# Optimization experiments

Measured on AMD Instinct MI355X. Metric: run time of the kernel, lower is better.

## Reference

```python
import jax, jax.numpy as jnp
import numpy as np

B, S, E, H = 4, 2048, 1024, 16
D = E // H  # key_size


def setup_inputs() -> dict:
    key = jax.random.key(0)
    ks = jax.random.split(key, 6)
    s = 1.0 / np.sqrt(E)
    return {
        "X": jax.random.normal(ks[0], (B, S, E), dtype=jnp.float32),
        "Wq": jax.random.uniform(ks[1], (E, E), jnp.float32, -s, s),
        "Wk": jax.random.uniform(ks[2], (E, E), jnp.float32, -s, s),
        "Wv": jax.random.uniform(ks[3], (E, E), jnp.float32, -s, s),
        "Wo": jax.random.uniform(ks[4], (E, E), jnp.float32, -s, s),
        "bo": jax.random.uniform(ks[5], (E,), jnp.float32, -s, s),
    }


def reference(X, Wq, Wk, Wv, Wo, bo):
    # Linear layers: y = x @ W^T (torch convention), no bias for q/k/v
    def split(x):  # [B,S,E] -> [B,H,S,D]
        return x.reshape(B, S, H, D).transpose(0, 2, 1, 3)

    q = split(X @ Wq.T)
    k = split(X @ Wk.T)
    v = split(X @ Wv.T)
    scale = jnp.asarray(np.sqrt(D), dtype=X.dtype)
    scores = jnp.einsum("bhqd,bhkd->bhqk", q, k) / scale
    probs = jax.nn.softmax(scores, axis=-1)
    ctx = jnp.einsum("bhqk,bhkd->bhqd", probs, v)
    out = ctx.transpose(0, 2, 1, 3).reshape(B, S, E)
    return out @ Wo.T + bo
```

## Files before the change

kernel.cpp:

```cpp
#include <hip/hip_runtime.h>
#include <hip/hip_bf16.h>

typedef short bf16x8 __attribute__((ext_vector_type(8)));
typedef float f32x4  __attribute__((ext_vector_type(4)));

__device__ __forceinline__ short f2bf(float f) {
    union { float f; unsigned u; } x; x.f = f;
    unsigned r = x.u + 0x7fffu + ((x.u >> 16) & 1u);
    return (short)(r >> 16);
}

__device__ __forceinline__ unsigned rbits(float f) {
    union { float f; unsigned u; } x; x.f = f;
    return x.u + 0x8000u;
}
__device__ __forceinline__ int pack2(float a, float b) {
    return (int)__builtin_amdgcn_perm(rbits(b), rbits(a), 0x07060302u);
}

__device__ __forceinline__ f32x4 mfma32k(bf16x8 a, bf16x8 b, f32x4 c) {
    return __builtin_amdgcn_mfma_f32_16x16x32_bf16(a, b, c, 0, 0, 0);
}

#define GLDS16(g, l)                                                            \
    __builtin_amdgcn_global_load_lds(                                           \
        (const __attribute__((address_space(1))) void*)(g),                     \
        (__attribute__((address_space(3))) void*)(l), 16, 0, 0)

static constexpr int Bb = 4, Ss = 2048, Ee = 1024, Hh = 16, Dd = 64;
static constexpr int Mrows = Bb * Ss;
static constexpr float CL2 = 0.1803368801111204f;

__global__ void cvt_all(const float* __restrict__ X,  const float* __restrict__ Wq,
                        const float* __restrict__ Wk, const float* __restrict__ Wv,
                        const float* __restrict__ Wo,
                        short* __restrict__ Xb, short* __restrict__ Wqk,
                        short* __restrict__ Wvb, short* __restrict__ Wob) {
    int bid = blockIdx.x;
    const float* src; short* dst; int off; float scale = 1.0f;
    if (bid < 8192) {
        src = X; dst = Xb; off = bid * 1024;
    } else {
        int wsel = (bid - 8192) >> 10;
        off = ((bid - 8192) & 1023) * 1024;
        if      (wsel == 0) { src = Wq; dst = Wqk;                scale = CL2; }
        else if (wsel == 1) { src = Wk; dst = Wqk + Ee * Ee; }
        else if (wsel == 2) { src = Wv; dst = Wvb; }
        else                { src = Wo; dst = Wob; }
    }
    int i = off + threadIdx.x * 4;
    float4 v = *(const float4*)(src + i);
    short4 o;
    o.x = f2bf(v.x * scale); o.y = f2bf(v.y * scale);
    o.z = f2bf(v.z * scale); o.w = f2bf(v.w * scale);
    *(short4*)(dst + i) = o;
}

__device__ __forceinline__ void gemm_pipe_256x128(
    short* lds, const short* hA, const short* hB,
    int wv, int lane16, int wn, int fsw0, int fsw1, int aoff,
    f32x4 (&acc)[8][2])
{
#define STG(gsrc, matOff, half, j, T, buf)                                      \
    GLDS16((gsrc) + ((half) * 128 + (j) * 64) * 1024 + (T) * 64,                \
           lds + (buf) * 32768 + (matOff) + (half) * 8192 + (j) * 4096 + wv * 512)

    STG(hA, 0,     0, 0, 0, 0); STG(hA, 0,     0, 1, 0, 0);
    STG(hA, 0,     1, 0, 0, 0); STG(hA, 0,     1, 1, 0, 0);
    STG(hB, 16384, 0, 0, 0, 0); STG(hB, 16384, 0, 1, 0, 0);
    STG(hA, 0,     0, 0, 1, 1); STG(hA, 0,     0, 1, 1, 1);
    asm volatile("s_waitcnt vmcnt(2)" ::: "memory");
    __builtin_amdgcn_s_barrier();

    const int bvoff = (wn * 32 + lane16) * 64;
    for (int T = 0; T < 16; ++T) {
        const int cur = T & 1, nxt = cur ^ 1;
        const short* sAc = lds + cur * 32768;
        const short* sBc = sAc + 16384;
        bf16x8 bb[2][2];
#pragma unroll
        for (int nj = 0; nj < 2; ++nj) {
            bb[nj][0] = *(const bf16x8*)(sBc + bvoff + nj * 1024 + fsw0);
            bb[nj][1] = *(const bf16x8*)(sBc + bvoff + nj * 1024 + fsw1);
        }
        bf16x8 a0, a1, a2, a3, a4, a5, a6, a7;
        a0 = *(const bf16x8*)(sAc + aoff + 0 * 1024 + fsw0);
        a1 = *(const bf16x8*)(sAc + aoff + 0 * 1024 + fsw1);
        a2 = *(const bf16x8*)(sAc + aoff + 1 * 1024 + fsw0);
        a3 = *(const bf16x8*)(sAc + aoff + 1 * 1024 + fsw1);
        a4 = *(const bf16x8*)(sAc + aoff + 2 * 1024 + fsw0);
        a5 = *(const bf16x8*)(sAc + aoff + 2 * 1024 + fsw1);
        a6 = *(const bf16x8*)(sAc + aoff + 3 * 1024 + fsw0);
        a7 = *(const bf16x8*)(sAc + aoff + 3 * 1024 + fsw1);
        if (T < 15) {
            STG(hA, 0,     1, 0, T + 1, nxt); STG(hA, 0,     1, 1, T + 1, nxt);
            STG(hB, 16384, 0, 0, T + 1, nxt); STG(hB, 16384, 0, 1, T + 1, nxt);
        }
        __builtin_amdgcn_s_barrier();
        __builtin_amdgcn_s_setprio(1);
#pragma unroll
        for (int nj = 0; nj < 2; ++nj) {
            acc[0][nj] = mfma32k(a0, bb[nj][0], acc[0][nj]);
            acc[0][nj] = mfma32k(a1, bb[nj][1], acc[0][nj]);
            acc[1][nj] = mfma32k(a2, bb[nj][0], acc[1][nj]);
            acc[1][nj] = mfma32k(a3, bb[nj][1], acc[1][nj]);
            acc[2][nj] = mfma32k(a4, bb[nj][0], acc[2][nj]);
            acc[2][nj] = mfma32k(a5, bb[nj][1], acc[2][nj]);
            acc[3][nj] = mfma32k(a6, bb[nj][0], acc[3][nj]);
            acc[3][nj] = mfma32k(a7, bb[nj][1], acc[3][nj]);
        }
        __builtin_amdgcn_s_setprio(0);
        __builtin_amdgcn_s_barrier();
        a0 = *(const bf16x8*)(sAc + aoff + 4 * 1024 + fsw0);
        a1 = *(const bf16x8*)(sAc + aoff + 4 * 1024 + fsw1);
        a2 = *(const bf16x8*)(sAc + aoff + 5 * 1024 + fsw0);
        a3 = *(const bf16x8*)(sAc + aoff + 5 * 1024 + fsw1);
        a4 = *(const bf16x8*)(sAc + aoff + 6 * 1024 + fsw0);
        a5 = *(const bf16x8*)(sAc + aoff + 6 * 1024 + fsw1);
        a6 = *(const bf16x8*)(sAc + aoff + 7 * 1024 + fsw0);
        a7 = *(const bf16x8*)(sAc + aoff + 7 * 1024 + fsw1);
        __builtin_amdgcn_s_barrier();
        __builtin_amdgcn_s_setprio(1);
#pragma unroll
        for (int nj = 0; nj < 2; ++nj) {
            acc[4][nj] = mfma32k(a0, bb[nj][0], acc[4][nj]);
            acc[4][nj] = mfma32k(a1, bb[nj][1], acc[4][nj]);
            acc[5][nj] = mfma32k(a2, bb[nj][0], acc[5][nj]);
            acc[5][nj] = mfma32k(a3, bb[nj][1], acc[5][nj]);
            acc[6][nj] = mfma32k(a4, bb[nj][0], acc[6][nj]);
            acc[6][nj] = mfma32k(a5, bb[nj][1], acc[6][nj]);
            acc[7][nj] = mfma32k(a6, bb[nj][0], acc[7][nj]);
            acc[7][nj] = mfma32k(a7, bb[nj][1], acc[7][nj]);
        }
        __builtin_amdgcn_s_setprio(0);
        __builtin_amdgcn_s_barrier();
        if (T < 14) {
            STG(hA, 0, 0, 0, T + 2, cur); STG(hA, 0, 0, 1, T + 2, cur);
            asm volatile("s_waitcnt vmcnt(2)" ::: "memory");
            __builtin_amdgcn_s_barrier();
        } else if (T == 14) {
            asm volatile("s_waitcnt vmcnt(0)" ::: "memory");
            __builtin_amdgcn_s_barrier();
        }
    }
#undef STG
}

__global__ __launch_bounds__(512, 2)
void gemm_fused(const short* __restrict__ A0, const short* __restrict__ B0,
                short* __restrict__ C0,
                const short* __restrict__ A1, const short* __restrict__ B1,
                short* __restrict__ C1) {
    __shared__ __align__(16) short lds[65536];
    const int t = threadIdx.x, l = t & 63, wv = t >> 6;
    const int lane16 = l & 15, quad = l >> 4;
    const int wm = wv >> 2, wn = wv & 3;

    int bid = blockIdx.x;
    int wg = (bid & 7) * 32 + (bid >> 3);
    const int bm = wg & 31, bn = wg >> 5;

    const int grow = t >> 3;
    const int lsl  = ((t & 7) ^ ((t >> 3) & 7)) * 8;
    const short* gA = A0 + (size_t)(bm * 256 + grow) * 1024 + lsl;
    const short* gB = B0 + (size_t)(bn * 256 + grow) * 1024 + lsl;

#define STAGE8(gsrc, matOff, half, j, T, buf)                                   \
    GLDS16((gsrc) + ((half) * 128 + (j) * 64) * 1024 + (T) * 64,                \
           lds + (buf) * 32768 + (matOff) + (half) * 8192 + (j) * 4096 + wv * 512)

    const int fsw0 = ((quad)     ^ (lane16 & 7)) * 8;
    const int fsw1 = ((quad + 4) ^ (lane16 & 7)) * 8;
    const int aoff = (wm * 128 + lane16) * 64;
    const int boff = (wn * 64  + lane16) * 64;

    f32x4 acc[8][4] = {};

    STAGE8(gA, 0,     0, 0, 0, 0); STAGE8(gA, 0,     0, 1, 0, 0);
    STAGE8(gA, 0,     1, 0, 0, 0); STAGE8(gA, 0,     1, 1, 0, 0);
    STAGE8(gB, 16384, 0, 0, 0, 0); STAGE8(gB, 16384, 0, 1, 0, 0);
    STAGE8(gB, 16384, 1, 0, 0, 0); STAGE8(gB, 16384, 1, 1, 0, 0);
    STAGE8(gA, 0,     0, 0, 1, 1); STAGE8(gA, 0,     0, 1, 1, 1);
    asm volatile("s_waitcnt vmcnt(2)" ::: "memory");
    __builtin_amdgcn_s_barrier();

#define ARD(MI0)                                                                \
    a0 = *(const bf16x8*)(sAc + aoff + (MI0) * 1024 + fsw0);                    \
    a1 = *(const bf16x8*)(sAc + aoff + (MI0) * 1024 + fsw1);                    \
    a2 = *(const bf16x8*)(sAc + aoff + ((MI0) + 1) * 1024 + fsw0);              \
    a3 = *(const bf16x8*)(sAc + aoff + ((MI0) + 1) * 1024 + fsw1);

#define MFQ(MI0)                                                                \
    __builtin_amdgcn_s_setprio(1);                                              \
    _Pragma("unroll")                                                           \
    for (int nj = 0; nj < 4; ++nj) {                                            \
        acc[MI0][nj]       = mfma32k(a0, bf[nj][0], acc[MI0][nj]);              \
        acc[MI0][nj]       = mfma32k(a1, bf[nj][1], acc[MI0][nj]);              \
        acc[(MI0) + 1][nj] = mfma32k(a2, bf[nj][0], acc[(MI0) + 1][nj]);        \
        acc[(MI0) + 1][nj] = mfma32k(a3, bf[nj][1], acc[(MI0) + 1][nj]);        \
    }                                                                           \
    __builtin_amdgcn_s_setprio(0);

    for (int T = 0; T < 16; ++T) {
        const int cur = T & 1, nxt = cur ^ 1;
        const short* sAc = lds + cur * 32768;
        const short* sBc = sAc + 16384;
        bf16x8 bf[4][2];
#pragma unroll
        for (int nj = 0; nj < 4; ++nj) {
            bf[nj][0] = *(const bf16x8*)(sBc + boff + nj * 1024 + fsw0);
            bf[nj][1] = *(const bf16x8*)(sBc + boff + nj * 1024 + fsw1);
        }
        bf16x8 a0, a1, a2, a3;
        ARD(0)
        if (T < 15) { STAGE8(gA, 0, 1, 0, T + 1, nxt); STAGE8(gA, 0, 1, 1, T + 1, nxt); }
        __builtin_amdgcn_s_barrier();
        MFQ(0)
        __builtin_amdgcn_s_barrier();
        ARD(2)
        if (T < 15) { STAGE8(gB, 16384, 0, 0, T + 1, nxt); STAGE8(gB, 16384, 0, 1, T + 1, nxt); }
        __builtin_amdgcn_s_barrier();
        MFQ(2)
        __builtin_amdgcn_s_barrier();
        ARD(4)
        if (T < 15) { STAGE8(gB, 16384, 1, 0, T + 1, nxt); STAGE8(gB, 16384, 1, 1, T + 1, nxt); }
        __builtin_amdgcn_s_barrier();
        MFQ(4)
        __builtin_amdgcn_s_barrier();
        ARD(6)
        __builtin_amdgcn_s_barrier();
        MFQ(6)
        __builtin_amdgcn_s_barrier();
        if (T < 14) {
            STAGE8(gA, 0, 0, 0, T + 2, cur); STAGE8(gA, 0, 0, 1, T + 2, cur);
            asm volatile("s_waitcnt vmcnt(2)" ::: "memory");
            __builtin_amdgcn_s_barrier();
        } else if (T == 14) {
            asm volatile("s_waitcnt vmcnt(0)" ::: "memory");
            __builtin_amdgcn_s_barrier();
        }
    }
#undef ARD
#undef MFQ
#undef STAGE8

#pragma unroll
    for (int mi = 0; mi < 8; ++mi)
#pragma unroll
        for (int nj = 0; nj < 4; ++nj) {
            int row = bm * 256 + wm * 128 + mi * 16 + quad * 4;
            int col = bn * 256 + wn * 64 + nj * 16 + lane16;
#pragma unroll
            for (int r = 0; r < 4; ++r)
                C0[(size_t)(row + r) * 2048 + col] = f2bf(acc[mi][nj][r]);
        }

    const int vbm = wg & 3, vbn = wg >> 2;
    const short* hA = A1 + (size_t)(vbm * 256 + grow) * 1024 + lsl;
    const short* hB = B1 + (size_t)(vbn * 128 + grow) * 1024 + lsl;
    f32x4 accB[8][2] = {};
    gemm_pipe_256x128(lds, hA, hB, wv, lane16, wn, fsw0, fsw1, aoff, accB);

    const int sEven = (lane16 >> 2) * 8 + (lane16 & 3);
#pragma unroll
    for (int mi = 0; mi < 8; ++mi)
#pragma unroll
        for (int nj = 0; nj < 2; ++nj) {
            int row = vbm * 256 + wm * 128 + mi * 16 + quad * 4;
            int col = vbn * 128 + wn * 32 + nj * 16 + lane16;
            col = (col & ~31) | (sEven + (nj & 1) * 4);
#pragma unroll
            for (int r = 0; r < 4; ++r)
                C1[(size_t)(row + r) * 8192 + col] = f2bf(accB[mi][nj][r]);
        }
}

__global__ __launch_bounds__(512, 2)
void gemm_out(const short* __restrict__ A, const short* __restrict__ Bm,
              float* __restrict__ C, const float* __restrict__ bias) {
    __shared__ __align__(16) short lds[65536];
    const int t = threadIdx.x, l = t & 63, wv = t >> 6;
    const int lane16 = l & 15, quad = l >> 4;
    const int wm = wv >> 2, wn = wv & 3;

    int bid = blockIdx.x;
    int wg = (bid & 7) * 32 + (bid >> 3);
    const int bm = wg >> 3, bn = wg & 7;

    const int grow = t >> 3;
    const int lsl  = ((t & 7) ^ ((t >> 3) & 7)) * 8;
    const short* hA = A  + (size_t)(bm * 256 + grow) * 1024 + lsl;
    const short* hB = Bm + (size_t)(bn * 128 + grow) * 1024 + lsl;

    const int fsw0 = ((quad)     ^ (lane16 & 7)) * 8;
    const int fsw1 = ((quad + 4) ^ (lane16 & 7)) * 8;
    const int aoff = (wm * 128 + lane16) * 64;

    f32x4 acc[8][2] = {};
    gemm_pipe_256x128(lds, hA, hB, wv, lane16, wn, fsw0, fsw1, aoff, acc);

#pragma unroll
    for (int mi = 0; mi < 8; ++mi)
#pragma unroll
        for (int nj = 0; nj < 2; ++nj) {
            int row = bm * 256 + wm * 128 + mi * 16 + quad * 4;
            int col = bn * 128 + wn * 32 + nj * 16 + lane16;
            float bv = bias[col];
#pragma unroll
            for (int r = 0; r < 4; ++r)
                C[(size_t)(row + r) * 1024 + col] = acc[mi][nj][r] + bv;
        }
}

__global__ __launch_bounds__(256, 4)
void attn_kernel(const short* __restrict__ QK, const short* __restrict__ VT,
                 short* __restrict__ CTX, int bh0) {
    __shared__ __align__(16) short sK[8192];
    __shared__ __align__(16) short sV[8192];
    const int t = threadIdx.x, w = t >> 6, l = t & 63;
    const int lane16 = l & 15, quad = l >> 4;
    const int bh = blockIdx.x + bh0, qt = blockIdx.y;
    const int b = bh >> 4, h = bh & 15;

    const int qx8 = (quad ^ ((lane16 >> 1) & 3)) * 8;

    const short* Qb = QK + ((size_t)(b * 2048 + qt * 128)) * 2048 + h * 64;
    const short* Vb = VT + ((size_t)(h * 64)) * 8192 + (size_t)b * 2048;
    const int ldsOff = (w * 64) * 8;

    int off_kq[4], off_v[4];
#pragma unroll
    for (int p = 0; p < 4; ++p) {
        int c = p * 256 + t;
        int sw = ((c & 3) ^ ((c >> 3) & 3)) * 8;
        off_kq[p] = ((c >> 2) & 127) * 2048 + (c >> 9) * 32 + sw;
        off_v[p]  = ((c >> 2) & 63) * 8192 + (c >> 8) * 32 + sw;
    }

#pragma unroll
    for (int p = 0; p < 4; ++p)
        GLDS16(Qb + off_kq[p], sK + p * 2048 + ldsOff);
    __syncthreads();
    bf16x8 qf[2][2];
#pragma unroll
    for (int mt = 0; mt < 2; ++mt)
#pragma unroll
        for (int ks = 0; ks < 2; ++ks)
            qf[mt][ks] = *(const bf16x8*)(sK + ks * 4096 + (w * 32 + mt * 16 + lane16) * 32 + qx8);
    __syncthreads();

    const short one = (short)0x3F80;
    const bf16x8 ONE8 = {one, one, one, one, one, one, one, one};
    f32x4 lacc[2] = {};
    f32x4 o[2][4] = {};

    const short* kptr = QK + ((size_t)(b * 2048)) * 2048 + 1024 + h * 64;
    const short* vptr = Vb;

    auto QKB = [&](int a, f32x4 (&sc)[2][2]) {
        __builtin_amdgcn_s_setprio(1);
#pragma unroll
        for (int sub = 0; sub < 2; ++sub) {
            int nt = a * 2 + sub;
            bf16x8 kf0 = *(const bf16x8*)(sK + (nt * 16 + lane16) * 32 + qx8);
            bf16x8 kf1 = *(const bf16x8*)(sK + 4096 + (nt * 16 + lane16) * 32 + qx8);
#pragma unroll
            for (int mt = 0; mt < 2; ++mt) {
                f32x4 z = {};
                z = mfma32k(kf0, qf[mt][0], z);
                z = mfma32k(kf1, qf[mt][1], z);
                sc[mt][sub] = z;
            }
        }
        __builtin_amdgcn_s_setprio(0);
    };
    auto PVB = [&](int a, f32x4 (&sc)[2][2]) {
        bf16x8 pf[2];
#pragma unroll
        for (int mt = 0; mt < 2; ++mt) {
            union { int i[4]; bf16x8 v; } u;
#pragma unroll
            for (int sub = 0; sub < 2; ++sub) {
                f32x4 e;
#pragma unroll
                for (int r = 0; r < 4; ++r)
                    e[r] = __builtin_amdgcn_exp2f(sc[mt][sub][r]);
                u.i[sub * 2]     = pack2(e[0], e[1]);
                u.i[sub * 2 + 1] = pack2(e[2], e[3]);
            }
            pf[mt] = u.v;
        }
        __builtin_amdgcn_s_setprio(1);
#pragma unroll
        for (int mt = 0; mt < 2; ++mt)
            lacc[mt] = mfma32k(pf[mt], ONE8, lacc[mt]);
#pragma unroll
        for (int dt = 0; dt < 4; ++dt) {
            bf16x8 vf = *(const bf16x8*)(sV + a * 2048 + (dt * 16 + lane16) * 32 + qx8);
#pragma unroll
            for (int mt = 0; mt < 2; ++mt)
                o[mt][dt] = mfma32k(pf[mt], vf, o[mt][dt]);
        }
        __builtin_amdgcn_s_setprio(0);
    };

    for (int kt = 0; kt < 16; ++kt) {
#pragma unroll
        for (int p = 0; p < 4; ++p)
            GLDS16(kptr + off_kq[p], sK + p * 2048 + ldsOff);
#pragma unroll
        for (int p = 0; p < 4; ++p)
            GLDS16(vptr + off_v[p], sV + p * 2048 + ldsOff);
        kptr += (size_t)128 * 2048;
        vptr += 128;
        __syncthreads();

        f32x4 scA[2][2], scB[2][2];
        QKB(0, scA);
        QKB(1, scB);  PVB(0, scA);
        QKB(2, scA);  PVB(1, scB);
        QKB(3, scB);  PVB(2, scA);
                      PVB(3, scB);
        __syncthreads();
    }

#pragma unroll
    for (int mt = 0; mt < 2; ++mt)
#pragma unroll
        for (int r = 0; r < 4; ++r) {
            float inv = 1.0f / lacc[mt][r];
            int row = b * 2048 + qt * 128 + w * 32 + mt * 16 + quad * 4 + r;
#pragma unroll
            for (int dt = 0; dt < 4; ++dt)
                CTX[(size_t)row * 1024 + h * 64 + dt * 16 + lane16] = f2bf(o[mt][dt][r] * inv);
        }
}

extern "C" void kernel_launch(void* const* d_in, const int* in_sizes, int n_in,
                              void* d_out, int out_size, void* d_ws, size_t ws_size,
                              hipStream_t stream) {
    const float* X  = (const float*)d_in[0];
    const float* Wq = (const float*)d_in[1];
    const float* Wk = (const float*)d_in[2];
    const float* Wv = (const float*)d_in[3];
    const float* Wo = (const float*)d_in[4];
    const float* bo = (const float*)d_in[5];
    float* out = (float*)d_out;

    char* ws = (char*)d_ws;
    constexpr size_t OFF_XB  = 0;
    constexpr size_t OFF_WQK = OFF_XB  + (size_t)Mrows * Ee * 2;
    constexpr size_t OFF_WV  = OFF_WQK + (size_t)2 * Ee * Ee * 2;
    constexpr size_t OFF_WO  = OFF_WV  + (size_t)Ee * Ee * 2;
    constexpr size_t OFF_QK  = OFF_WO  + (size_t)Ee * Ee * 2;
    constexpr size_t OFF_VT  = OFF_QK  + (size_t)Mrows * 2048 * 2;
    constexpr size_t OFF_CTX = OFF_VT  + (size_t)Ee * Mrows * 2;
    short* Xb   = (short*)(ws + OFF_XB);
    short* Wqk  = (short*)(ws + OFF_WQK);
    short* Wvb  = (short*)(ws + OFF_WV);
    short* Wob  = (short*)(ws + OFF_WO);
    short* QKb  = (short*)(ws + OFF_QK);
    short* VTb  = (short*)(ws + OFF_VT);
    short* CTX  = (short*)(ws + OFF_CTX);

    cvt_all<<<12288, 256, 0, stream>>>(X, Wq, Wk, Wv, Wo, Xb, Wqk, Wvb, Wob);

    gemm_fused<<<256, 512, 0, stream>>>(Xb, Wqk, QKb, Wvb, Xb, VTb);

    attn_kernel<<<dim3(Bb * Hh, Ss / 128), 256, 0, stream>>>(QKb, VTb, CTX, 0);

    gemm_out<<<256, 512, 0, stream>>>(CTX, Wob, out, bo);
}
```

Before: 248.7 us.

## Reshape 256x128 GEMM warp tiling to 4x2 and split attention launch in two

Changes the per-warp tile in the 256x128 GEMM pipeline from 128x32 (8x2 MFMA tiles) to 64x64 (4x4 tiles). Each warp now does fewer LDS A-fragment reads and more B-fragment reuse per stage, giving a more balanced operand load. The epilogues of the fused V projection and the output GEMM are remapped to match. The attention launch is also split into two launches of 32 batch-heads each, which adds launch overhead and has no clear speed rationale.

```diff
diff --git a/kernel.cpp b/kernel.cpp
--- a/kernel.cpp
+++ b/kernel.cpp
@@ -58,8 +58,8 @@
 
 __device__ __forceinline__ void gemm_pipe_256x128(
     short* lds, const short* hA, const short* hB,
-    int wv, int lane16, int wn, int fsw0, int fsw1, int aoff,
-    f32x4 (&acc)[8][2])
+    int wv, int lane16, int fsw0, int fsw1,
+    f32x4 (&acc)[4][4])
 {
 #define STG(gsrc, matOff, half, j, T, buf)                                      \
     GLDS16((gsrc) + ((half) * 128 + (j) * 64) * 1024 + (T) * 64,                \
@@ -72,26 +72,25 @@
     asm volatile("s_waitcnt vmcnt(2)" ::: "memory");
     __builtin_amdgcn_s_barrier();
 
-    const int bvoff = (wn * 32 + lane16) * 64;
+    const int wm2 = wv & 3, wn2 = wv >> 2;
+    const int aoff = (wm2 * 64 + lane16) * 64;
+    const int boff = (wn2 * 64 + lane16) * 64;
+
     for (int T = 0; T < 16; ++T) {
         const int cur = T & 1, nxt = cur ^ 1;
         const short* sAc = lds + cur * 32768;
         const short* sBc = sAc + 16384;
-        bf16x8 bb[2][2];
-#pragma unroll
-        for (int nj = 0; nj < 2; ++nj) {
-            bb[nj][0] = *(const bf16x8*)(sBc + bvoff + nj * 1024 + fsw0);
-            bb[nj][1] = *(const bf16x8*)(sBc + bvoff + nj * 1024 + fsw1);
-        }
-        bf16x8 a0, a1, a2, a3, a4, a5, a6, a7;
+        bf16x8 bb[4][2];
+#pragma unroll
+        for (int nj = 0; nj < 4; ++nj) {
+            bb[nj][0] = *(const bf16x8*)(sBc + boff + nj * 1024 + fsw0);
+            bb[nj][1] = *(const bf16x8*)(sBc + boff + nj * 1024 + fsw1);
+        }
+        bf16x8 a0, a1, a2, a3;
         a0 = *(const bf16x8*)(sAc + aoff + 0 * 1024 + fsw0);
         a1 = *(const bf16x8*)(sAc + aoff + 0 * 1024 + fsw1);
         a2 = *(const bf16x8*)(sAc + aoff + 1 * 1024 + fsw0);
         a3 = *(const bf16x8*)(sAc + aoff + 1 * 1024 + fsw1);
-        a4 = *(const bf16x8*)(sAc + aoff + 2 * 1024 + fsw0);
-        a5 = *(const bf16x8*)(sAc + aoff + 2 * 1024 + fsw1);
-        a6 = *(const bf16x8*)(sAc + aoff + 3 * 1024 + fsw0);
-        a7 = *(const bf16x8*)(sAc + aoff + 3 * 1024 + fsw1);
         if (T < 15) {
             STG(hA, 0,     1, 0, T + 1, nxt); STG(hA, 0,     1, 1, T + 1, nxt);
             STG(hB, 16384, 0, 0, T + 1, nxt); STG(hB, 16384, 0, 1, T + 1, nxt);
@@ -99,38 +98,26 @@
         __builtin_amdgcn_s_barrier();
         __builtin_amdgcn_s_setprio(1);
 #pragma unroll
-        for (int nj = 0; nj < 2; ++nj) {
+        for (int nj = 0; nj < 4; ++nj) {
             acc[0][nj] = mfma32k(a0, bb[nj][0], acc[0][nj]);
             acc[0][nj] = mfma32k(a1, bb[nj][1], acc[0][nj]);
             acc[1][nj] = mfma32k(a2, bb[nj][0], acc[1][nj]);
             acc[1][nj] = mfma32k(a3, bb[nj][1], acc[1][nj]);
-            acc[2][nj] = mfma32k(a4, bb[nj][0], acc[2][nj]);
-            acc[2][nj] = mfma32k(a5, bb[nj][1], acc[2][nj]);
-            acc[3][nj] = mfma32k(a6, bb[nj][0], acc[3][nj]);
-            acc[3][nj] = mfma32k(a7, bb[nj][1], acc[3][nj]);
         }
         __builtin_amdgcn_s_setprio(0);
         __builtin_amdgcn_s_barrier();
-        a0 = *(const bf16x8*)(sAc + aoff + 4 * 1024 + fsw0);
-        a1 = *(const bf16x8*)(sAc + aoff + 4 * 1024 + fsw1);
-        a2 = *(const bf16x8*)(sAc + aoff + 5 * 1024 + fsw0);
-        a3 = *(const bf16x8*)(sAc + aoff + 5 * 1024 + fsw1);
-        a4 = *(const bf16x8*)(sAc + aoff + 6 * 1024 + fsw0);
-        a5 = *(const bf16x8*)(sAc + aoff + 6 * 1024 + fsw1);
-        a6 = *(const bf16x8*)(sAc + aoff + 7 * 1024 + fsw0);
-        a7 = *(const bf16x8*)(sAc + aoff + 7 * 1024 + fsw1);
+        a0 = *(const bf16x8*)(sAc + aoff + 2 * 1024 + fsw0);
+        a1 = *(const bf16x8*)(sAc + aoff + 2 * 1024 + fsw1);
+        a2 = *(const bf16x8*)(sAc + aoff + 3 * 1024 + fsw0);
+        a3 = *(const bf16x8*)(sAc + aoff + 3 * 1024 + fsw1);
         __builtin_amdgcn_s_barrier();
         __builtin_amdgcn_s_setprio(1);
 #pragma unroll
-        for (int nj = 0; nj < 2; ++nj) {
-            acc[4][nj] = mfma32k(a0, bb[nj][0], acc[4][nj]);
-            acc[4][nj] = mfma32k(a1, bb[nj][1], acc[4][nj]);
-            acc[5][nj] = mfma32k(a2, bb[nj][0], acc[5][nj]);
-            acc[5][nj] = mfma32k(a3, bb[nj][1], acc[5][nj]);
-            acc[6][nj] = mfma32k(a4, bb[nj][0], acc[6][nj]);
-            acc[6][nj] = mfma32k(a5, bb[nj][1], acc[6][nj]);
-            acc[7][nj] = mfma32k(a6, bb[nj][0], acc[7][nj]);
-            acc[7][nj] = mfma32k(a7, bb[nj][1], acc[7][nj]);
+        for (int nj = 0; nj < 4; ++nj) {
+            acc[2][nj] = mfma32k(a0, bb[nj][0], acc[2][nj]);
+            acc[2][nj] = mfma32k(a1, bb[nj][1], acc[2][nj]);
+            acc[3][nj] = mfma32k(a2, bb[nj][0], acc[3][nj]);
+            acc[3][nj] = mfma32k(a3, bb[nj][1], acc[3][nj]);
         }
         __builtin_amdgcn_s_setprio(0);
         __builtin_amdgcn_s_barrier();
@@ -258,16 +245,17 @@
     const int vbm = wg & 3, vbn = wg >> 2;
     const short* hA = A1 + (size_t)(vbm * 256 + grow) * 1024 + lsl;
     const short* hB = B1 + (size_t)(vbn * 128 + grow) * 1024 + lsl;
-    f32x4 accB[8][2] = {};
-    gemm_pipe_256x128(lds, hA, hB, wv, lane16, wn, fsw0, fsw1, aoff, accB);
-
+    f32x4 accB[4][4] = {};
+    gemm_pipe_256x128(lds, hA, hB, wv, lane16, fsw0, fsw1, accB);
+
+    const int wm2 = wv & 3, wn2 = wv >> 2;
     const int sEven = (lane16 >> 2) * 8 + (lane16 & 3);
 #pragma unroll
-    for (int mi = 0; mi < 8; ++mi)
-#pragma unroll
-        for (int nj = 0; nj < 2; ++nj) {
-            int row = vbm * 256 + wm * 128 + mi * 16 + quad * 4;
-            int col = vbn * 128 + wn * 32 + nj * 16 + lane16;
+    for (int mi = 0; mi < 4; ++mi)
+#pragma unroll
+        for (int nj = 0; nj < 4; ++nj) {
+            int row = vbm * 256 + wm2 * 64 + mi * 16 + quad * 4;
+            int col = vbn * 128 + wn2 * 64 + nj * 16 + lane16;
             col = (col & ~31) | (sEven + (nj & 1) * 4);
 #pragma unroll
             for (int r = 0; r < 4; ++r)
@@ -281,7 +269,6 @@
     __shared__ __align__(16) short lds[65536];
     const int t = threadIdx.x, l = t & 63, wv = t >> 6;
     const int lane16 = l & 15, quad = l >> 4;
-    const int wm = wv >> 2, wn = wv & 3;
 
     int bid = blockIdx.x;
     int wg = (bid & 7) * 32 + (bid >> 3);
@@ -294,17 +281,17 @@
 
     const int fsw0 = ((quad)     ^ (lane16 & 7)) * 8;
     const int fsw1 = ((quad + 4) ^ (lane16 & 7)) * 8;
-    const int aoff = (wm * 128 + lane16) * 64;
-
-    f32x4 acc[8][2] = {};
-    gemm_pipe_256x128(lds, hA, hB, wv, lane16, wn, fsw0, fsw1, aoff, acc);
-
-#pragma unroll
-    for (int mi = 0; mi < 8; ++mi)
-#pragma unroll
-        for (int nj = 0; nj < 2; ++nj) {
-            int row = bm * 256 + wm * 128 + mi * 16 + quad * 4;
-            int col = bn * 128 + wn * 32 + nj * 16 + lane16;
+
+    f32x4 acc[4][4] = {};
+    gemm_pipe_256x128(lds, hA, hB, wv, lane16, fsw0, fsw1, acc);
+
+    const int wm2 = wv & 3, wn2 = wv >> 2;
+#pragma unroll
+    for (int mi = 0; mi < 4; ++mi)
+#pragma unroll
+        for (int nj = 0; nj < 4; ++nj) {
+            int row = bm * 256 + wm2 * 64 + mi * 16 + quad * 4;
+            int col = bn * 128 + wn2 * 64 + nj * 16 + lane16;
             float bv = bias[col];
 #pragma unroll
             for (int r = 0; r < 4; ++r)
@@ -467,7 +454,8 @@
 
     gemm_fused<<<256, 512, 0, stream>>>(Xb, Wqk, QKb, Wvb, Xb, VTb);
 
-    attn_kernel<<<dim3(Bb * Hh, Ss / 128), 256, 0, stream>>>(QKb, VTb, CTX, 0);
+    attn_kernel<<<dim3(32, Ss / 128), 256, 0, stream>>>(QKb, VTb, CTX, 0);
+    attn_kernel<<<dim3(32, Ss / 128), 256, 0, stream>>>(QKb, VTb, CTX, 32);
 
     gemm_out<<<256, 512, 0, stream>>>(CTX, Wob, out, bo);
 }
```

Measured after the change: 243.0 us. 1.02x faster.
